# Kernel tuning notes

Measured on AMD Instinct MI355X. Metric: run time of the kernel, lower is better.

Reference implementation:

```python
import jax, jax.numpy as jnp
import numpy as np

B, T, F, H = 128, 1024, 64, 256


def _lstm_cell(x, h, c, W_ih, W_hh, b):
    # x: [B,F], h,c: [B,H]; gate order i,f,g,o (PyTorch convention)
    gates = x @ W_ih.T + h @ W_hh.T + b  # [B,4H]
    i, f, g, o = jnp.split(gates, 4, axis=-1)
    i, f, o = jax.nn.sigmoid(i), jax.nn.sigmoid(f), jax.nn.sigmoid(o)
    g = jnp.tanh(g)
    c = f * c + i * g
    h = o * jnp.tanh(c)
    return h, c


def setup_inputs() -> dict:
    key = jax.random.key(0)
    ks = jax.random.split(key, 10)
    s = 1.0 / np.sqrt(H)
    inp = {
        "ts_batch": jax.random.normal(ks[0], (B, T, F), jnp.float32),
        "W_ih_enc": jax.random.uniform(ks[1], (4 * H, F), jnp.float32, -s, s),
        "W_hh_enc": jax.random.uniform(ks[2], (4 * H, H), jnp.float32, -s, s),
        "b_enc": jax.random.uniform(ks[3], (4 * H,), jnp.float32, -s, s),
        "W_ih_dec": jax.random.uniform(ks[4], (4 * H, F), jnp.float32, -s, s),
        "W_hh_dec": jax.random.uniform(ks[5], (4 * H, H), jnp.float32, -s, s),
        "b_dec": jax.random.uniform(ks[6], (4 * H,), jnp.float32, -s, s),
        "W_out": jax.random.uniform(ks[7], (F, H), jnp.float32, -s, s),
        "b_out": jax.random.uniform(ks[8], (F,), jnp.float32, -s, s),
    }
    return inp


def reference(ts_batch, W_ih_enc, W_hh_enc, b_enc, W_ih_dec, W_hh_dec, b_dec, W_out, b_out):
    batch = ts_batch.shape[0]
    hidden = W_hh_enc.shape[1]
    xs = jnp.swapaxes(ts_batch, 0, 1)  # [T,B,F]

    # ---- encoder: full-sequence LSTM, keep only final (h,c) ----
    def enc_step(carry, x):
        h, c = carry
        h, c = _lstm_cell(x, h, c, W_ih_enc, W_hh_enc, b_enc)
        return (h, c), None

    h0 = jnp.zeros((batch, hidden), ts_batch.dtype)
    (h, c), _ = jax.lax.scan(enc_step, (h0, h0), xs)

    # ---- decoder: iterate timesteps in reverse; emit projection of the
    # hidden state BEFORE consuming the input at that step (training branch) ----
    def dec_step(carry, x):
        h, c = carry
        out = h @ W_out.T + b_out  # [B,F]
        h, c = _lstm_cell(x, h, c, W_ih_dec, W_hh_dec, b_dec)
        return (h, c), out

    _, outs_rev = jax.lax.scan(dec_step, (h, c), xs[::-1])  # [T,B,F], reversed time
    return jnp.swapaxes(outs_rev[::-1], 0, 1)  # [B,T,F]
```

## Files before the change

kernel.cpp:

```cpp
#include <hip/hip_runtime.h>
#include <hip/hip_bf16.h>


#define Bb 128
#define Tt 1024
#define Ff 64
#define Hh 256

typedef _Float16 h16;
typedef __attribute__((ext_vector_type(8))) _Float16 h16x8;
typedef __attribute__((ext_vector_type(4))) float f32x4;
typedef __attribute__((ext_vector_type(4))) unsigned int u32x4;
typedef unsigned long long u64;
typedef unsigned int u32;

#define WENC_OFF 0
#define WDEC_OFF 327680
#define WOUT_OFF 655360
#define FLAGS_BYTE_OFF 1474560
#define TAGHB_BYTE_OFF 1475584

__device__ __forceinline__ float fast_sigmoid(float x) {
  float e = __expf(-fabsf(x));
  float s = __builtin_amdgcn_rcpf(1.f + e);
  return x >= 0.f ? s : 1.f - s;
}
__device__ __forceinline__ float fast_tanh(float x) {
  float e = __expf(-2.f * fabsf(x));
  float r = (1.f - e) * __builtin_amdgcn_rcpf(1.f + e);
  return x >= 0.f ? r : -r;
}
__device__ __forceinline__ h16x8 pack16(u64 lo, u64 hi) {
  union { u64 u[2]; h16x8 v; } x;
  x.u[0] = lo; x.u[1] = hi;
  return x.v;
}
__device__ __forceinline__ u64 detag4(u32x4 g) {
  u32 lo = (g[0] & 0xFFFFu) | (g[1] << 16);
  u32 hi = (g[2] & 0xFFFFu) | (g[3] << 16);
  return (u64)lo | ((u64)hi << 32);
}

__global__ void lstm_prep(const float* __restrict__ Wih_e, const float* __restrict__ Whh_e,
                          const float* __restrict__ Wih_d, const float* __restrict__ Whh_d,
                          const float* __restrict__ Wout, h16* __restrict__ ws16,
                          unsigned int* __restrict__ flags) {
  int e = blockIdx.x * 256 + threadIdx.x;
  if (e < 256) flags[e] = 0u;
  if (e < 65536) {
    u32* tag32 = flags + 256;
    tag32[e] = 0xFFFF0000u;
  }
  if (e < 655360) {
    int r = e;
    const float* Wih = Wih_e; const float* Whh = Whh_e;
    int off = WENC_OFF;
    if (r >= 327680) { r -= 327680; Wih = Wih_d; Whh = Whh_d; off = WDEC_OFF; }
    int j    = r & 7;
    int lane = (r >> 3) & 63;
    int kt   = (r >> 9) % 10;
    int tmp  = (r >> 9) / 10;
    int nt   = tmp & 7;
    int w    = (tmp >> 3) & 3;
    int q    = tmp >> 5;
    int g = nt >> 1, ct = nt & 1;
    int col = q * 128 + w * 32 + ct * 16 + (lane & 15);
    int row = g * 256 + col;
    int k = kt * 32 + (lane >> 4) * 8 + j;
    float v = (k < 64) ? Wih[row * 64 + k] : Whh[row * 256 + (k - 64)];
    ws16[off + r] = (h16)v;
  } else if (e < 655360 + 16384) {
    int r = e - 655360;
    int j    = r & 7;
    int lane = (r >> 3) & 63;
    int kt   = (r >> 9) & 7;
    int wt   = (r >> 12) & 1;
    int q    = (r >> 13) & 1;
    int f = q * 32 + wt * 16 + (lane & 15);
    int k = kt * 32 + (lane >> 4) * 8 + j;
    ws16[WOUT_OFF + r] = (h16)Wout[f * 256 + k];
  }
}

#define MFMA_KT(kt) do {                                                         \
    acc[0] = __builtin_amdgcn_mfma_f32_16x16x32_f16(a[kt], wf[0][kt], acc[0], 0, 0, 0); \
    acc[1] = __builtin_amdgcn_mfma_f32_16x16x32_f16(a[kt], wf[1][kt], acc[1], 0, 0, 0); \
    acc[2] = __builtin_amdgcn_mfma_f32_16x16x32_f16(a[kt], wf[2][kt], acc[2], 0, 0, 0); \
    acc[3] = __builtin_amdgcn_mfma_f32_16x16x32_f16(a[kt], wf[3][kt], acc[3], 0, 0, 0); \
    acc[4] = __builtin_amdgcn_mfma_f32_16x16x32_f16(a[kt], wf[4][kt], acc[4], 0, 0, 0); \
    acc[5] = __builtin_amdgcn_mfma_f32_16x16x32_f16(a[kt], wf[5][kt], acc[5], 0, 0, 0); \
    acc[6] = __builtin_amdgcn_mfma_f32_16x16x32_f16(a[kt], wf[6][kt], acc[6], 0, 0, 0); \
    acc[7] = __builtin_amdgcn_mfma_f32_16x16x32_f16(a[kt], wf[7][kt], acc[7], 0, 0, 0); \
  } while (0)

#define LOADRND(SC) do {                                                         \
    asm volatile(                                                                \
        "global_load_dwordx4 %0, %8, off " SC "\n\t"                             \
        "global_load_dwordx4 %1, %8, off offset:16 " SC "\n\t"                   \
        "global_load_dwordx4 %2, %8, off offset:128 " SC "\n\t"                  \
        "global_load_dwordx4 %3, %8, off offset:144 " SC "\n\t"                  \
        "global_load_dwordx4 %4, %8, off offset:256 " SC "\n\t"                  \
        "global_load_dwordx4 %5, %8, off offset:272 " SC "\n\t"                  \
        "global_load_dwordx4 %6, %8, off offset:384 " SC "\n\t"                  \
        "global_load_dwordx4 %7, %8, off offset:400 " SC "\n\t"                  \
        "s_waitcnt vmcnt(0)"                                                     \
        : "=&v"(g0), "=&v"(g1), "=&v"(g2), "=&v"(g3),                            \
          "=&v"(g4), "=&v"(g5), "=&v"(g6), "=&v"(g7)                             \
        : "v"(tbp)                                                               \
        : "memory");                                                             \
  } while (0)

__global__ __launch_bounds__(256, 1) void lstm_main(
    const float* __restrict__ ts,
    const float* __restrict__ b_enc, const float* __restrict__ b_dec,
    const float* __restrict__ b_out,
    const h16* __restrict__ wsW, u64* __restrict__ tagbuf,
    float* __restrict__ out) {
  const int tid = threadIdx.x;
  const int wg = blockIdx.x;
  const int grp = wg & 7, q = wg >> 3;
  const int w = tid >> 6, lane = tid & 63;
  const int n16 = lane & 15, quad = lane >> 4;
  const int b0 = grp * 16;
  const int partner = wg ^ 8;

  __shared__ __align__(16) h16 xh[2][16][328];
  __shared__ h16x8 woutLds[1024];

  h16x8 wf[8][10];
  {
    const h16x8* wsrc = (const h16x8*)(wsW + WENC_OFF);
#pragma unroll
    for (int nt = 0; nt < 8; ++nt)
#pragma unroll
      for (int kt = 0; kt < 10; ++kt)
        wf[nt][kt] = wsrc[(((q * 4 + w) * 8 + nt) * 10 + kt) * 64 + lane];
  }
  float bias8[8];
#pragma unroll
  for (int nt = 0; nt < 8; ++nt) {
    int g = nt >> 1, ct = nt & 1;
    bias8[nt] = b_enc[g * 256 + q * 128 + w * 32 + ct * 16 + n16];
  }
  const float bo = b_out[q * 32 + w * 16 + n16];

  float c8[8];
#pragma unroll
  for (int i = 0; i < 8; ++i) c8[i] = 0.f;

  for (int i = tid; i < 16 * 264; i += 256) {
    int m = i / 264;
    xh[0][m][64 + (i - m * 264)] = (h16)0.f;
  }
  const int m_x = tid >> 4, ks_x = (tid & 15) * 4;
  {
    const f32x4 xv0 = *(const f32x4*)(ts + ((size_t)(b0 + m_x) * Tt + 0) * Ff + ks_x);
#pragma unroll
    for (int u = 0; u < 4; ++u) xh[0][m_x][ks_x + u] = (h16)xv0[u];
  }
  __syncthreads();

  const int jb = (n16 * 16 + quad) * 2;

  for (int t = 0; t < 2048; ++t) {
    const int nb = t & 1, nxt = nb ^ 1;
    const bool dec = (t >= 1024);

    if (t == 1024) {
      const h16x8* wsrc2 = (const h16x8*)(wsW + WDEC_OFF);
#pragma unroll
      for (int nt = 0; nt < 8; ++nt)
#pragma unroll
        for (int kt = 0; kt < 10; ++kt)
          wf[nt][kt] = wsrc2[(((q * 4 + w) * 8 + nt) * 10 + kt) * 64 + lane];
#pragma unroll
      for (int nt = 0; nt < 8; ++nt) {
        int g = nt >> 1, ct = nt & 1;
        bias8[nt] = b_dec[g * 256 + q * 128 + w * 32 + ct * 16 + n16];
      }
      const h16x8* wo = (const h16x8*)(wsW + WOUT_OFF) + q * 1024;
      for (int i = tid; i < 1024; i += 256) woutLds[i] = wo[i];
      __syncthreads();
    }

    h16x8 a[10];
    const h16* xrow = &xh[nb][n16][0];
    a[0] = *(const h16x8*)(xrow + 0 * 32 + quad * 8);
    a[1] = *(const h16x8*)(xrow + 1 * 32 + quad * 8);
    if (q == 0) {
      a[2] = *(const h16x8*)(xrow + 2 * 32 + quad * 8);
      a[3] = *(const h16x8*)(xrow + 3 * 32 + quad * 8);
      a[4] = *(const h16x8*)(xrow + 4 * 32 + quad * 8);
      a[5] = *(const h16x8*)(xrow + 5 * 32 + quad * 8);
    } else {
      a[6] = *(const h16x8*)(xrow + 6 * 32 + quad * 8);
      a[7] = *(const h16x8*)(xrow + 7 * 32 + quad * 8);
      a[8] = *(const h16x8*)(xrow + 8 * 32 + quad * 8);
      a[9] = *(const h16x8*)(xrow + 9 * 32 + quad * 8);
    }

    f32x4 xv;
#pragma unroll
    for (int u = 0; u < 4; ++u) xv[u] = 0.f;
    if (t + 1 < 2048) {
      int xi = (t + 1 < 1024) ? (t + 1) : (2047 - (t + 1));
      xv = *(const f32x4*)(ts + ((size_t)(b0 + m_x) * Tt + xi) * Ff + ks_x);
    }

    f32x4 acc[8];
#pragma unroll
    for (int nt = 0; nt < 8; ++nt) {
      f32x4 v; v[0] = bias8[nt]; v[1] = bias8[nt]; v[2] = bias8[nt]; v[3] = bias8[nt];
      acc[nt] = v;
    }
    MFMA_KT(0); MFMA_KT(1);
    if (q == 0) { MFMA_KT(2); MFMA_KT(3); MFMA_KT(4); MFMA_KT(5); }
    else        { MFMA_KT(6); MFMA_KT(7); MFMA_KT(8); MFMA_KT(9); }

    if (t > 0) {
      const char* tbp = (const char*)(tagbuf + ((size_t)partner * 2 + nxt) * 1024)
                        + (size_t)jb * 16;
      u32x4 g0, g1, g2, g3, g4, g5, g6, g7;
      const u32 tgt = (u32)t;
      int round = 0;
      for (;;) {
        if (round >= 2 && (round & 1) == 0) { LOADRND("sc0 sc1"); }
        else                                { LOADRND("sc0"); }
        u32 bad = 0u;
#pragma unroll
        for (int j = 0; j < 4; ++j) {
          bad |= (g0[j] >> 16) ^ tgt; bad |= (g1[j] >> 16) ^ tgt;
          bad |= (g2[j] >> 16) ^ tgt; bad |= (g3[j] >> 16) ^ tgt;
          bad |= (g4[j] >> 16) ^ tgt; bad |= (g5[j] >> 16) ^ tgt;
          bad |= (g6[j] >> 16) ^ tgt; bad |= (g7[j] >> 16) ^ tgt;
        }
        if (bad == 0u) break;
        ++round;
      }
      u64 d0 = detag4(g0), d1 = detag4(g1), d2 = detag4(g2), d3 = detag4(g3);
      u64 d4 = detag4(g4), d5 = detag4(g5), d6 = detag4(g6), d7 = detag4(g7);
      if (q == 0) {
        a[6] = pack16(d0, d1); a[7] = pack16(d2, d3);
        a[8] = pack16(d4, d5); a[9] = pack16(d6, d7);
        MFMA_KT(6); MFMA_KT(7); MFMA_KT(8); MFMA_KT(9);
      } else {
        a[2] = pack16(d0, d1); a[3] = pack16(d2, d3);
        a[4] = pack16(d4, d5); a[5] = pack16(d6, d7);
        MFMA_KT(2); MFMA_KT(3); MFMA_KT(4); MFMA_KT(5);
      }
    }

    h16 hv[8];
#pragma unroll
    for (int ct = 0; ct < 2; ++ct)
#pragma unroll
      for (int r = 0; r < 4; ++r) {
        float i_ = fast_sigmoid(acc[0 + ct][r]);
        float f_ = fast_sigmoid(acc[2 + ct][r]);
        float g_ = fast_tanh(acc[4 + ct][r]);
        float o_ = fast_sigmoid(acc[6 + ct][r]);
        float cv = f_ * c8[ct * 4 + r] + i_ * g_;
        c8[ct * 4 + r] = cv;
        hv[ct * 4 + r] = (h16)(o_ * fast_tanh(cv));
      }

#pragma unroll
    for (int ct = 0; ct < 2; ++ct)
#pragma unroll
      for (int r = 0; r < 4; ++r) {
        int m = quad * 4 + r;
        int colLocal = w * 32 + ct * 16 + n16;
        xh[nxt][m][64 + q * 128 + colLocal] = hv[ct * 4 + r];
      }
    if (t + 1 < 2048) {
#pragma unroll
      for (int u = 0; u < 4; ++u) xh[nxt][m_x][ks_x + u] = (h16)xv[u];
    }

    __syncthreads();

    if (t < 2047) {
      const u32 tagw = (u32)(t + 1) << 16;
      const char* pbb = (const char*)(tagbuf + ((size_t)wg * 2 + nb) * 1024);
      u64 v0 = *(const u64*)(&xh[nxt][tid >> 5][64 + q * 128 + (tid & 31) * 4]);
      u64 v1 = *(const u64*)(&xh[nxt][(tid + 256) >> 5][64 + q * 128 + (tid & 31) * 4]);
      u32x4 s0, s1;
      {
        u32 lo = (u32)v0, hi = (u32)(v0 >> 32);
        s0[0] = tagw | (lo & 0xFFFFu); s0[1] = tagw | (lo >> 16);
        s0[2] = tagw | (hi & 0xFFFFu); s0[3] = tagw | (hi >> 16);
      }
      {
        u32 lo = (u32)v1, hi = (u32)(v1 >> 32);
        s1[0] = tagw | (lo & 0xFFFFu); s1[1] = tagw | (lo >> 16);
        s1[2] = tagw | (hi & 0xFFFFu); s1[3] = tagw | (hi >> 16);
      }
      const char* p0 = pbb + (size_t)tid * 16;
      const char* p1 = pbb + (size_t)(tid + 256) * 16;
      asm volatile(
          "global_store_dwordx4 %0, %2, off sc0 sc1\n\t"
          "global_store_dwordx4 %1, %3, off sc0 sc1"
          :: "v"(p0), "v"(p1), "v"(s0), "v"(s1)
          : "memory");
    }

    if (dec && w < 2) {
      f32x4 ao; ao[0] = bo; ao[1] = bo; ao[2] = bo; ao[3] = bo;
#pragma unroll
      for (int kt = 0; kt < 8; ++kt)
        ao = __builtin_amdgcn_mfma_f32_16x16x32_f16(a[2 + kt], woutLds[(w * 8 + kt) * 64 + lane], ao, 0, 0, 0);
      int tpos = 2047 - t;
      int f = q * 32 + w * 16 + n16;
#pragma unroll
      for (int r = 0; r < 4; ++r) {
        int m = quad * 4 + r;
        out[((size_t)(b0 + m) * Tt + tpos) * Ff + f] = ao[r];
      }
    }
  }
}

extern "C" void kernel_launch(void* const* d_in, const int* in_sizes, int n_in,
                              void* d_out, int out_size, void* d_ws, size_t ws_size,
                              hipStream_t stream) {
  const float* ts  = (const float*)d_in[0];
  const float* Wie = (const float*)d_in[1];
  const float* Whe = (const float*)d_in[2];
  const float* be  = (const float*)d_in[3];
  const float* Wid = (const float*)d_in[4];
  const float* Whd = (const float*)d_in[5];
  const float* bd  = (const float*)d_in[6];
  const float* Wo  = (const float*)d_in[7];
  const float* bo  = (const float*)d_in[8];

  h16* ws16 = (h16*)d_ws;
  unsigned int* flags = (unsigned int*)((char*)d_ws + FLAGS_BYTE_OFF);
  u64* tagbuf = (u64*)((char*)d_ws + TAGHB_BYTE_OFF);
  float* out = (float*)d_out;

  lstm_prep<<<2624, 256, 0, stream>>>(Wie, Whe, Wid, Whd, Wo, ws16, flags);
  lstm_main<<<16, 256, 0, stream>>>(ts, be, bd, bo, ws16, tagbuf, out);
}
```

Measured before the change: 9.581 ms.

## Speculatively prefetch partner hidden-state tags and next input one step early

```diff
diff --git a/kernel.cpp b/kernel.cpp
--- a/kernel.cpp
+++ b/kernel.cpp
@@ -93,20 +93,36 @@
     acc[7] = __builtin_amdgcn_mfma_f32_16x16x32_f16(a[kt], wf[7][kt], acc[7], 0, 0, 0); \
   } while (0)
 
-#define LOADRND(SC) do {                                                         \
+#define SPECISSUE(PTR) do {                                                      \
     asm volatile(                                                                \
-        "global_load_dwordx4 %0, %8, off " SC "\n\t"                             \
-        "global_load_dwordx4 %1, %8, off offset:16 " SC "\n\t"                   \
-        "global_load_dwordx4 %2, %8, off offset:128 " SC "\n\t"                  \
-        "global_load_dwordx4 %3, %8, off offset:144 " SC "\n\t"                  \
-        "global_load_dwordx4 %4, %8, off offset:256 " SC "\n\t"                  \
-        "global_load_dwordx4 %5, %8, off offset:272 " SC "\n\t"                  \
-        "global_load_dwordx4 %6, %8, off offset:384 " SC "\n\t"                  \
-        "global_load_dwordx4 %7, %8, off offset:400 " SC "\n\t"                  \
+        "global_load_dwordx4 %0, %8, off sc0 sc1\n\t"                            \
+        "global_load_dwordx4 %1, %8, off offset:16 sc0 sc1\n\t"                  \
+        "global_load_dwordx4 %2, %8, off offset:128 sc0 sc1\n\t"                 \
+        "global_load_dwordx4 %3, %8, off offset:144 sc0 sc1\n\t"                 \
+        "global_load_dwordx4 %4, %8, off offset:256 sc0 sc1\n\t"                 \
+        "global_load_dwordx4 %5, %8, off offset:272 sc0 sc1\n\t"                 \
+        "global_load_dwordx4 %6, %8, off offset:384 sc0 sc1\n\t"                 \
+        "global_load_dwordx4 %7, %8, off offset:400 sc0 sc1"                     \
+        : "=&v"(g0), "=&v"(g1), "=&v"(g2), "=&v"(g3),                            \
+          "=&v"(g4), "=&v"(g5), "=&v"(g6), "=&v"(g7)                             \
+        : "v"(PTR)                                                               \
+        : "memory");                                                             \
+  } while (0)
+
+#define LOADRND_IC(PTR) do {                                                     \
+    asm volatile(                                                                \
+        "global_load_dwordx4 %0, %8, off sc0 sc1\n\t"                            \
+        "global_load_dwordx4 %1, %8, off offset:16 sc0 sc1\n\t"                  \
+        "global_load_dwordx4 %2, %8, off offset:128 sc0 sc1\n\t"                 \
+        "global_load_dwordx4 %3, %8, off offset:144 sc0 sc1\n\t"                 \
+        "global_load_dwordx4 %4, %8, off offset:256 sc0 sc1\n\t"                 \
+        "global_load_dwordx4 %5, %8, off offset:272 sc0 sc1\n\t"                 \
+        "global_load_dwordx4 %6, %8, off offset:384 sc0 sc1\n\t"                 \
+        "global_load_dwordx4 %7, %8, off offset:400 sc0 sc1\n\t"                 \
         "s_waitcnt vmcnt(0)"                                                     \
         : "=&v"(g0), "=&v"(g1), "=&v"(g2), "=&v"(g3),                            \
           "=&v"(g4), "=&v"(g5), "=&v"(g6), "=&v"(g7)                             \
-        : "v"(tbp)                                                               \
+        : "v"(PTR)                                                               \
         : "memory");                                                             \
   } while (0)
 
@@ -161,6 +177,10 @@
   __syncthreads();
 
   const int jb = (n16 * 16 + quad) * 2;
+
+  f32x4 xv = *(const f32x4*)(ts + ((size_t)(b0 + m_x) * Tt + 1) * Ff + ks_x);
+
+  u32x4 g0, g1, g2, g3, g4, g5, g6, g7;
 
   for (int t = 0; t < 2048; ++t) {
     const int nb = t & 1, nxt = nb ^ 1;
@@ -199,14 +219,6 @@
       a[9] = *(const h16x8*)(xrow + 9 * 32 + quad * 8);
     }
 
-    f32x4 xv;
-#pragma unroll
-    for (int u = 0; u < 4; ++u) xv[u] = 0.f;
-    if (t + 1 < 2048) {
-      int xi = (t + 1 < 1024) ? (t + 1) : (2047 - (t + 1));
-      xv = *(const f32x4*)(ts + ((size_t)(b0 + m_x) * Tt + xi) * Ff + ks_x);
-    }
-
     f32x4 acc[8];
 #pragma unroll
     for (int nt = 0; nt < 8; ++nt) {
@@ -218,14 +230,12 @@
     else        { MFMA_KT(6); MFMA_KT(7); MFMA_KT(8); MFMA_KT(9); }
 
     if (t > 0) {
+      asm volatile("s_waitcnt vmcnt(0)" ::: "memory");
+      __builtin_amdgcn_sched_barrier(0);
       const char* tbp = (const char*)(tagbuf + ((size_t)partner * 2 + nxt) * 1024)
                         + (size_t)jb * 16;
-      u32x4 g0, g1, g2, g3, g4, g5, g6, g7;
       const u32 tgt = (u32)t;
-      int round = 0;
       for (;;) {
-        if (round >= 2 && (round & 1) == 0) { LOADRND("sc0 sc1"); }
-        else                                { LOADRND("sc0"); }
         u32 bad = 0u;
 #pragma unroll
         for (int j = 0; j < 4; ++j) {
@@ -235,7 +245,8 @@
           bad |= (g6[j] >> 16) ^ tgt; bad |= (g7[j] >> 16) ^ tgt;
         }
         if (bad == 0u) break;
-        ++round;
+        __builtin_amdgcn_s_sleep(1);
+        LOADRND_IC(tbp);
       }
       u64 d0 = detag4(g0), d1 = detag4(g1), d2 = detag4(g2), d3 = detag4(g3);
       u64 d4 = detag4(g4), d5 = detag4(g5), d6 = detag4(g6), d7 = detag4(g7);
@@ -316,6 +327,18 @@
         int m = quad * 4 + r;
         out[((size_t)(b0 + m) * Tt + tpos) * Ff + f] = ao[r];
       }
+    }
+
+    if (t + 2 < 2048) {
+      int u2 = t + 2;
+      int xi = (u2 < 1024) ? u2 : (2047 - u2);
+      xv = *(const f32x4*)(ts + ((size_t)(b0 + m_x) * Tt + xi) * Ff + ks_x);
+    }
+
+    if (t < 2047) {
+      const char* tbs = (const char*)(tagbuf + ((size_t)partner * 2 + nb) * 1024)
+                        + (size_t)jb * 16;
+      SPECISSUE(tbs);
     }
   }
 }
```

Measured after the change: 9.910 ms. 1.03x slower.
